# Kernel tuning notes

Measured on AMD Instinct MI355X. Metric: run time of the kernel, lower is better.

Reference implementation:

```python
import jax, jax.numpy as jnp
import numpy as np

N = 50000      # nodes
E = 1600000    # edges
F_IN = 128     # input_dim
H = 160        # hidden_dim
G = 512        # graphs in batch
C = 2          # num_classes
EPS = 1e-5     # BatchNorm eps


def setup_inputs() -> dict:
    key = jax.random.key(0)
    ks = jax.random.split(key, 12)
    x = jax.random.normal(ks[0], (N, F_IN), jnp.float32)
    edge_index = jax.random.randint(ks[1], (2, E), 0, N, dtype=jnp.int32)
    batch = jnp.sort(jax.random.randint(ks[2], (N,), 0, G, dtype=jnp.int32))

    def lin(k, fi, fo):
        s = 1.0 / np.sqrt(fi)
        kw, kb = jax.random.split(k)
        W = jax.random.uniform(kw, (fi, fo), jnp.float32, -s, s)
        b = jax.random.uniform(kb, (fo,), jnp.float32, -s, s)
        return W, b

    W1, b1 = lin(ks[3], F_IN, H)
    W2, b2 = lin(ks[4], H, H)
    W3, b3 = lin(ks[5], H, H)
    Wc1, bc1 = lin(ks[6], H, H // 2)
    Wc2, bc2 = lin(ks[7], H // 2, C)

    def bn(k):
        k1, k2, k3, k4 = jax.random.split(k, 4)
        gamma = jax.random.uniform(k1, (H,), jnp.float32, 0.5, 1.5)
        beta = jax.random.normal(k2, (H,), jnp.float32) * 0.1
        mean = jax.random.normal(k3, (H,), jnp.float32) * 0.1
        var = jax.random.uniform(k4, (H,), jnp.float32, 0.5, 1.5)
        return gamma, beta, mean, var

    g1, be1, m1, v1 = bn(ks[8])
    g2, be2, m2, v2 = bn(ks[9])
    g3, be3, m3, v3 = bn(ks[10])

    return dict(x=x, edge_index=edge_index, batch=batch,
                W1=W1, b1=b1, W2=W2, b2=b2, W3=W3, b3=b3,
                g1=g1, be1=be1, m1=m1, v1=v1,
                g2=g2, be2=be2, m2=m2, v2=v2,
                g3=g3, be3=be3, m3=m3, v3=v3,
                Wc1=Wc1, bc1=bc1, Wc2=Wc2, bc2=bc2)


def gcn_conv(x, W, b, src, dst):
    """PyG GCNConv: symmetric deg normalization with self-loops; lin -> aggregate -> +bias."""
    n = x.shape[0]
    h = x @ W                                   # [N, H]
    loop = jnp.arange(n, dtype=src.dtype)
    s = jnp.concatenate([src, loop])            # self-loops appended
    d = jnp.concatenate([dst, loop])
    deg = jax.ops.segment_sum(jnp.ones_like(d, jnp.float32), d, num_segments=n)
    inv = jnp.where(deg > 0, jax.lax.rsqrt(deg), 0.0)
    msg = h[s] * (inv[s] * inv[d])[:, None]     # [E+N, H] gather + norm
    return jax.ops.segment_sum(msg, d, num_segments=n) + b


def bn_eval(x, gamma, beta, mean, var):
    return (x - mean) * jax.lax.rsqrt(var + EPS) * gamma + beta


def reference(x, edge_index, batch, W1, b1, W2, b2, W3, b3,
              g1, be1, m1, v1, g2, be2, m2, v2, g3, be3, m3, v3,
              Wc1, bc1, Wc2, bc2):
    src, dst = edge_index[0], edge_index[1]
    # eval mode: dropout is identity, BN uses running stats
    h = jax.nn.relu(bn_eval(gcn_conv(x, W1, b1, src, dst), g1, be1, m1, v1))
    h = jax.nn.relu(bn_eval(gcn_conv(h, W2, b2, src, dst), g2, be2, m2, v2))
    h = jax.nn.relu(bn_eval(gcn_conv(h, W3, b3, src, dst), g3, be3, m3, v3))
    # global mean pool over graph ids
    sums = jax.ops.segment_sum(h, batch, num_segments=G)
    cnt = jax.ops.segment_sum(jnp.ones((h.shape[0],), jnp.float32), batch, num_segments=G)
    pooled = sums / jnp.clip(cnt, 1.0)[:, None]
    # MLP head
    z = jax.nn.relu(pooled @ Wc1 + bc1)
    return z @ Wc2 + bc2
```

## Files before the change

### kernel.cpp

```cpp
#include <hip/hip_runtime.h>

#define N_NODES   50000
#define N_EDGES   1600000
#define FDIM_IN   128
#define HDIM      160
#define N_GRAPHS  512
#define BN_EPS    1e-5f
#define NBKT_MAX  256
#define BKT_SH    8
#define HIST_BLOCKS 128

typedef short  frag8 __attribute__((ext_vector_type(8)));
typedef float  facc4 __attribute__((ext_vector_type(4)));


__device__ __forceinline__ unsigned short f2bf(float f) {
    unsigned int u = __float_as_uint(f);
    return (unsigned short)((u + 0x7FFFu + ((u >> 16) & 1u)) >> 16);
}

__device__ __forceinline__ unsigned int pack2(float lo, float hi) {
    return (unsigned int)f2bf(lo) | ((unsigned int)f2bf(hi) << 16);
}

__device__ __forceinline__ void addpk(float* acc, uint4 r) {
    acc[0] += __uint_as_float(r.x << 16);
    acc[1] += __uint_as_float(r.x & 0xFFFF0000u);
    acc[2] += __uint_as_float(r.y << 16);
    acc[3] += __uint_as_float(r.y & 0xFFFF0000u);
    acc[4] += __uint_as_float(r.z << 16);
    acc[5] += __uint_as_float(r.z & 0xFFFF0000u);
    acc[6] += __uint_as_float(r.w << 16);
    acc[7] += __uint_as_float(r.w & 0xFFFF0000u);
}


__global__ __launch_bounds__(256) void coarse_hist_kernel(const int* __restrict__ dst,
                                                          int* __restrict__ cg, int E) {
    __shared__ int h[NBKT_MAX];
    int tid = threadIdx.x;
    if (tid < NBKT_MAX) h[tid] = 0;
    __syncthreads();
    for (int e = blockIdx.x * 256 + tid; e < E; e += gridDim.x * 256)
        atomicAdd(&h[dst[e] >> BKT_SH], 1);
    __syncthreads();
    if (tid < NBKT_MAX) cg[blockIdx.x * NBKT_MAX + tid] = h[tid];
}


struct PrepArgs {
    const float *b, *g, *be, *m, *v;
    float *sc, *sh;
};

__global__ __launch_bounds__(256) void setup_kernel(const int* __restrict__ cg,
                                                    int* __restrict__ bucket_base,
                                                    int* __restrict__ bucket_cursor,
                                                    PrepArgs a0, PrepArgs a1, PrepArgs a2,
                                                    const float* __restrict__ W1,
                                                    const float* __restrict__ W2,
                                                    const float* __restrict__ W3,
                                                    unsigned short* __restrict__ o1,
                                                    unsigned short* __restrict__ o2,
                                                    unsigned short* __restrict__ o3) {
    int bid = blockIdx.x;
    int t = threadIdx.x;
    if (bid == 0) {
        __shared__ int h[NBKT_MAX];
        __shared__ int total;
        if (t < NBKT_MAX) {
            int s = 0;
            for (int b = 0; b < HIST_BLOCKS; ++b) s += cg[b * NBKT_MAX + t];
            h[t] = s;
        }
        __syncthreads();
        if (t == 0) {
            int run = 0;
            for (int i = 0; i < NBKT_MAX; ++i) { int c = h[i]; h[i] = run; run += c; }
            total = run;
        }
        __syncthreads();
        if (t < NBKT_MAX) {
            bucket_base[t] = h[t];
            bucket_cursor[t] = h[t];
        }
        if (t == 0) bucket_base[NBKT_MAX] = total;
    } else if (bid <= 3) {
        PrepArgs a = (bid == 1) ? a0 : (bid == 2) ? a1 : a2;
        if (t < HDIM) {
            float s = a.g[t] * rsqrtf(a.v[t] + BN_EPS);
            a.sc[t] = s;
            a.sh[t] = (a.b[t] - a.m[t]) * s + a.be[t];
        }
    } else {
        int i = (bid - 4) * 256 + t;
        const float* W;
        unsigned short* o;
        if (i < 128 * 160)                 { W = W1; o = o1; }
        else if (i < 128 * 160 + 160 * 160) { W = W2; o = o2; i -= 128 * 160; }
        else if (i < 128 * 160 + 2 * 160 * 160) { W = W3; o = o3; i -= 128 * 160 + 160 * 160; }
        else return;
        int j = i & 7;
        int l = (i >> 3) & 63;
        int u = (i >> 9) % 10;
        int tt = i / 5120;
        int k = tt * 32 + (l >> 4) * 8 + j;
        int nn = u * 16 + (l & 15);
        o[i] = f2bf(W[k * 160 + nn]);
    }
}

__global__ __launch_bounds__(256) void part_kernel(const int* __restrict__ src,
                                                   const int* __restrict__ dst,
                                                   int* __restrict__ bucket_cursor,
                                                   unsigned int* __restrict__ pairs, int E) {
    __shared__ int bcnt[NBKT_MAX], bbase[NBKT_MAX], lc[NBKT_MAX];
    int tid = threadIdx.x;
    int per = (E + gridDim.x - 1) / gridDim.x;
    int beg = blockIdx.x * per;
    int end = min(beg + per, E);
    if (tid < NBKT_MAX) { bcnt[tid] = 0; lc[tid] = 0; }
    __syncthreads();
    for (int e = beg + tid; e < end; e += 256)
        atomicAdd(&bcnt[dst[e] >> BKT_SH], 1);
    __syncthreads();
    if (tid < NBKT_MAX)
        bbase[tid] = bcnt[tid] ? atomicAdd(&bucket_cursor[tid], bcnt[tid]) : 0;
    __syncthreads();
    for (int e = beg + tid; e < end; e += 256) {
        int d = dst[e];
        int b = d >> BKT_SH;
        int pos = bbase[b] + atomicAdd(&lc[b], 1);
        pairs[pos] = ((unsigned int)src[e] << BKT_SH) | (unsigned int)(d & (NBKT_MAX - 1));
    }
}

__global__ __launch_bounds__(1024) void bucket_csr_kernel(const unsigned int* __restrict__ pairs,
                                                          const int* __restrict__ bucket_base,
                                                          int* __restrict__ row_off,
                                                          float* __restrict__ inv,
                                                          int* __restrict__ ssrc,
                                                          const float* __restrict__ x,
                                                          unsigned short* __restrict__ xs,
                                                          int n) {
    __shared__ int h[NBKT_MAX];
    __shared__ int ws[4];
    __shared__ float sinv[NBKT_MAX];
    int tid = threadIdx.x;
    int b = blockIdx.x;
    int node0 = b << BKT_SH;
    int beg = bucket_base[b], end = bucket_base[b + 1];
    if (tid < NBKT_MAX) h[tid] = 0;
    __syncthreads();
    for (int j = beg + tid; j < end; j += 1024)
        atomicAdd(&h[pairs[j] & (NBKT_MAX - 1)], 1);
    __syncthreads();
    int cntv = (tid < NBKT_MAX) ? h[tid] : 0;
    __syncthreads();
    int lane = tid & 63, wid = tid >> 6;
    int incl = cntv;
    #pragma unroll
    for (int off = 1; off < 64; off <<= 1) {
        int u = __shfl_up(incl, off);
        if (lane >= off) incl += u;
    }
    if (tid < NBKT_MAX && lane == 63) ws[wid] = incl;
    __syncthreads();
    if (tid == 0) {
        int r = 0;
        #pragma unroll
        for (int i = 0; i < 4; ++i) { int t = ws[i]; ws[i] = r; r += t; }
    }
    __syncthreads();
    int excl = (tid < NBKT_MAX) ? (ws[wid] + incl - cntv) : 0;
    if (tid < NBKT_MAX) {
        float iv = rsqrtf((float)(cntv + 1));
        int node = node0 + tid;
        if (node < n) {
            row_off[node] = beg + excl;
            inv[node] = iv;
        }
        sinv[tid] = iv;
        h[tid] = excl;
    }
    if (tid == 0 && (node0 + NBKT_MAX) >= n) row_off[n] = end;
    __syncthreads();
    for (int j = beg + tid; j < end; j += 1024) {
        unsigned int p = pairs[j];
        int pos = beg + atomicAdd(&h[p & (NBKT_MAX - 1)], 1);
        ssrc[pos] = (int)(p >> BKT_SH);
    }
    for (int idx = tid; idx < NBKT_MAX * 32; idx += 1024) {
        int nd = node0 + (idx >> 5);
        if (nd < n) {
            float w = sinv[idx >> 5];
            float4 v = ((const float4*)x)[(size_t)nd * 32 + (idx & 31)];
            ushort4 o;
            o.x = f2bf(v.x * w); o.y = f2bf(v.y * w);
            o.z = f2bf(v.z * w); o.w = f2bf(v.w * w);
            ((ushort4*)xs)[(size_t)nd * 32 + (idx & 31)] = o;
        }
    }
}


template <int C>
__global__ __launch_bounds__(256) void agg_grp_kernel(const unsigned short* __restrict__ in_s,
                                                      const float* __restrict__ inv,
                                                      const int* __restrict__ row_off,
                                                      const int* __restrict__ ssrc,
                                                      unsigned short* __restrict__ out, int n) {
    constexpr int LPR = C / 8;
    constexpr int G   = 64 / LPR;
    constexpr int RB  = C * 2;
    int wave = threadIdx.x >> 6;
    int lane = threadIdx.x & 63;
    int node = blockIdx.x * 4 + wave;
    if (node >= n) return;
    int g  = lane / LPR;
    int cl = lane - g * LPR;
    bool act = g < G;
    int beg = row_off[node], end = row_off[node + 1];
    const char* base = (const char*)in_s;
    int lb = cl * 16;

    float acc[8];
    #pragma unroll
    for (int i = 0; i < 8; ++i) acc[i] = 0.f;

    if (g == 0) {
        uint4 r = *(const uint4*)(base + (size_t)node * RB + lb);
        addpk(acc, r);
    }

    int e = act ? beg + g : end;
    for (; e + G < end; e += 2 * G) {
        int s0 = ssrc[e], s1 = ssrc[e + G];
        uint4 r0 = *(const uint4*)(base + (size_t)s0 * RB + lb);
        uint4 r1 = *(const uint4*)(base + (size_t)s1 * RB + lb);
        addpk(acc, r0);
        addpk(acc, r1);
    }
    if (e < end) {
        uint4 r = *(const uint4*)(base + (size_t)ssrc[e] * RB + lb);
        addpk(acc, r);
    }

    if (G == 4) {
        #pragma unroll
        for (int i = 0; i < 8; ++i) acc[i] += __shfl(acc[i], lane + 32);
        #pragma unroll
        for (int i = 0; i < 8; ++i) acc[i] += __shfl(acc[i], lane + 16);
    } else {
        #pragma unroll
        for (int i = 0; i < 8; ++i) {
            float a = __shfl(acc[i], lane + 20);
            float b = __shfl(acc[i], lane + 40);
            acc[i] += a + b;
        }
    }

    if (lane < LPR) {
        float wi = inv[node];
        uint4 o;
        o.x = pack2(acc[0] * wi, acc[1] * wi);
        o.y = pack2(acc[2] * wi, acc[3] * wi);
        o.z = pack2(acc[4] * wi, acc[5] * wi);
        o.w = pack2(acc[6] * wi, acc[7] * wi);
        *(uint4*)((char*)out + (size_t)node * RB + lb) = o;
    }
}


template <int K, int OUTMODE>
__global__ __launch_bounds__(256) void mfma_gemm_kernel(const unsigned short* __restrict__ A,
                                                        const unsigned short* __restrict__ Bp,
                                                        const float* __restrict__ sc,
                                                        const float* __restrict__ sh,
                                                        const float* __restrict__ inv,
                                                        float* __restrict__ CoutF,
                                                        unsigned short* __restrict__ CoutB,
                                                        int n) {
    constexpr int KT = K / 32;
    constexpr int BQ = K * 20;
    __shared__ uint4 Bs[BQ];
    int tid = threadIdx.x;
    for (int i = tid; i < BQ; i += 256) Bs[i] = ((const uint4*)Bp)[i];

    int wave = tid >> 6, lane = tid & 63;
    int m = lane & 15, q = lane >> 4;
    int row0 = blockIdx.x * 128 + wave * 16;
    int row1 = row0 + 64;

    int ar0 = row0 + m; ar0 = (ar0 < n) ? ar0 : (n - 1);
    int ar1 = row1 + m; ar1 = (ar1 < n) ? ar1 : (n - 1);
    const frag8* A0 = (const frag8*)(A + (size_t)ar0 * K);
    const frag8* A1 = (const frag8*)(A + (size_t)ar1 * K);
    const frag8* Bf = (const frag8*)Bs;

    facc4 acc0[10], acc1[10];
    #pragma unroll
    for (int u = 0; u < 10; ++u) {
        acc0[u] = (facc4){0.f, 0.f, 0.f, 0.f};
        acc1[u] = (facc4){0.f, 0.f, 0.f, 0.f};
    }

    __syncthreads();

    #pragma unroll
    for (int t = 0; t < KT; ++t) {
        frag8 af0 = A0[t * 4 + q];
        frag8 af1 = A1[t * 4 + q];
        #pragma unroll
        for (int u = 0; u < 10; ++u) {
            frag8 bf = Bf[(t * 10 + u) * 64 + lane];
            acc0[u] = __builtin_amdgcn_mfma_f32_16x16x32_bf16(af0, bf, acc0[u], 0, 0, 0);
            acc1[u] = __builtin_amdgcn_mfma_f32_16x16x32_bf16(af1, bf, acc1[u], 0, 0, 0);
        }
    }

    #pragma unroll
    for (int u = 0; u < 10; ++u) {
        int c = u * 16 + m;
        float scv = sc[c], shv = sh[c];
        #pragma unroll
        for (int r = 0; r < 4; ++r) {
            int rr = row0 + q * 4 + r;
            if (rr < n) {
                float v = fmaxf(acc0[u][r] * scv + shv, 0.f);
                if (OUTMODE == 1) CoutB[(size_t)rr * 160 + c] = f2bf(v * inv[rr]);
                else              CoutF[(size_t)rr * 160 + c] = v;
            }
            int rr1 = row1 + q * 4 + r;
            if (rr1 < n) {
                float v = fmaxf(acc1[u][r] * scv + shv, 0.f);
                if (OUTMODE == 1) CoutB[(size_t)rr1 * 160 + c] = f2bf(v * inv[rr1]);
                else              CoutF[(size_t)rr1 * 160 + c] = v;
            }
        }
    }
}


__global__ __launch_bounds__(256) void pool_head_kernel(const float* __restrict__ h,
                                                        const int* __restrict__ batch,
                                                        const float* __restrict__ Wc1,
                                                        const float* __restrict__ bc1,
                                                        const float* __restrict__ Wc2,
                                                        const float* __restrict__ bc2,
                                                        float* __restrict__ out, int n) {
    __shared__ float4 part[6][40];
    __shared__ float pooled[160];
    __shared__ float z[80];
    __shared__ int range[2];
    int g = blockIdx.x;
    int t = threadIdx.x;
    if (t < 2) {
        int target = g + t;
        int lo = 0, hi = n;
        while (lo < hi) {
            int mid = (lo + hi) >> 1;
            if (batch[mid] < target) lo = mid + 1; else hi = mid;
        }
        range[t] = lo;
    }
    __syncthreads();
    int lo = range[0], hi = range[1];
    int sub = t / 40, c4 = t - sub * 40;
    if (sub < 6) {
        float4 a = {0.f, 0.f, 0.f, 0.f};
        for (int r = lo + sub; r < hi; r += 6) {
            float4 v = ((const float4*)(h + (size_t)r * 160))[c4];
            a.x += v.x; a.y += v.y; a.z += v.z; a.w += v.w;
        }
        part[sub][c4] = a;
    }
    __syncthreads();
    if (t < 40) {
        float4 s = {0.f, 0.f, 0.f, 0.f};
        #pragma unroll
        for (int i = 0; i < 6; ++i) {
            float4 p = part[i][t];
            s.x += p.x; s.y += p.y; s.z += p.z; s.w += p.w;
        }
        float ic = 1.f / fmaxf((float)(hi - lo), 1.f);
        pooled[t * 4 + 0] = s.x * ic;
        pooled[t * 4 + 1] = s.y * ic;
        pooled[t * 4 + 2] = s.z * ic;
        pooled[t * 4 + 3] = s.w * ic;
    }
    __syncthreads();
    if (t < 80) {
        float s = bc1[t];
        for (int k = 0; k < 160; ++k) s += pooled[k] * Wc1[k * 80 + t];
        z[t] = fmaxf(s, 0.f);
    }
    __syncthreads();
    if (t < 2) {
        float s = bc2[t];
        for (int k = 0; k < 80; ++k) s += z[k] * Wc2[k * 2 + t];
        out[g * 2 + t] = s;
    }
}


static inline size_t align256(size_t x) { return (x + 255) & ~(size_t)255; }

extern "C" void kernel_launch(void* const* d_in, const int* in_sizes, int n_in,
                              void* d_out, int out_size, void* d_ws, size_t ws_size,
                              hipStream_t stream) {
    const float* x   = (const float*)d_in[0];
    const int* ei    = (const int*)d_in[1];
    const int* batch = (const int*)d_in[2];
    const float* W1  = (const float*)d_in[3];
    const float* b1  = (const float*)d_in[4];
    const float* W2  = (const float*)d_in[5];
    const float* b2  = (const float*)d_in[6];
    const float* W3  = (const float*)d_in[7];
    const float* b3  = (const float*)d_in[8];
    const float* g1  = (const float*)d_in[9];
    const float* be1 = (const float*)d_in[10];
    const float* m1  = (const float*)d_in[11];
    const float* v1  = (const float*)d_in[12];
    const float* g2  = (const float*)d_in[13];
    const float* be2 = (const float*)d_in[14];
    const float* m2  = (const float*)d_in[15];
    const float* v2  = (const float*)d_in[16];
    const float* g3  = (const float*)d_in[17];
    const float* be3 = (const float*)d_in[18];
    const float* m3  = (const float*)d_in[19];
    const float* v3  = (const float*)d_in[20];
    const float* Wc1 = (const float*)d_in[21];
    const float* bc1 = (const float*)d_in[22];
    const float* Wc2 = (const float*)d_in[23];
    const float* bc2 = (const float*)d_in[24];
    float* out = (float*)d_out;

    const int N = in_sizes[2];
    const int E = in_sizes[1] / 2;
    const int* src = ei;
    const int* dst = ei + E;

    char* w = (char*)d_ws;
    int*   row_off = (int*)w;             w += align256((size_t)(N + 1) * 4);
    float* inv     = (float*)w;           w += align256((size_t)N * 4);
    int*   ssrc    = (int*)w;             w += align256((size_t)E * 4);
    unsigned int* pairs = (unsigned int*)w; w += align256((size_t)E * 4);
    int*   cg      = (int*)w;             w += align256((size_t)HIST_BLOCKS * NBKT_MAX * 4);
    int*   bucket_base   = (int*)w;       w += align256((size_t)(NBKT_MAX + 1) * 4);
    int*   bucket_cursor = (int*)w;       w += align256((size_t)NBKT_MAX * 4);
    float* scsh    = (float*)w;           w += align256((size_t)6 * HDIM * 4);
    unsigned short* W1p = (unsigned short*)w;  w += align256((size_t)FDIM_IN * HDIM * 2);
    unsigned short* W2p = (unsigned short*)w;  w += align256((size_t)HDIM * HDIM * 2);
    unsigned short* W3p = (unsigned short*)w;  w += align256((size_t)HDIM * HDIM * 2);
    unsigned short* bufA_bf = (unsigned short*)w;  w += align256((size_t)N * HDIM * 2);
    char* regionR = w;
    unsigned short* xs_bf = (unsigned short*)regionR;
    unsigned short* hs_bf = (unsigned short*)(regionR + align256((size_t)N * FDIM_IN * 2));
    float* bufB = (float*)regionR;
    float* sc1 = scsh, *sh1 = scsh + 160, *sc2 = scsh + 320, *sh2 = scsh + 480,
         * sc3 = scsh + 640, *sh3 = scsh + 800;

    coarse_hist_kernel<<<HIST_BLOCKS, 256, 0, stream>>>(dst, cg, E);

    PrepArgs pa0 = {b1, g1, be1, m1, v1, sc1, sh1};
    PrepArgs pa1 = {b2, g2, be2, m2, v2, sc2, sh2};
    PrepArgs pa2 = {b3, g3, be3, m3, v3, sc3, sh3};
    int packTotal = 128 * 160 + 2 * 160 * 160;
    int setupBlocks = 4 + (packTotal + 255) / 256;
    setup_kernel<<<setupBlocks, 256, 0, stream>>>(cg, bucket_base, bucket_cursor,
                                                  pa0, pa1, pa2, W1, W2, W3, W1p, W2p, W3p);

    part_kernel<<<256, 256, 0, stream>>>(src, dst, bucket_cursor, pairs, E);
    int nbkt = (N + NBKT_MAX - 1) >> BKT_SH;
    bucket_csr_kernel<<<nbkt, 1024, 0, stream>>>(pairs, bucket_base, row_off, inv, ssrc, x, xs_bf, N);

    int gAgg = (N + 3) / 4;
    int gGemm = (N + 127) / 128;

    agg_grp_kernel<128><<<gAgg, 256, 0, stream>>>(xs_bf, inv, row_off, ssrc, bufA_bf, N);
    mfma_gemm_kernel<128, 1><<<gGemm, 256, 0, stream>>>(bufA_bf, W1p, sc1, sh1, inv, nullptr, hs_bf, N);
    agg_grp_kernel<160><<<gAgg, 256, 0, stream>>>(hs_bf, inv, row_off, ssrc, bufA_bf, N);
    mfma_gemm_kernel<160, 1><<<gGemm, 256, 0, stream>>>(bufA_bf, W2p, sc2, sh2, inv, nullptr, hs_bf, N);
    agg_grp_kernel<160><<<gAgg, 256, 0, stream>>>(hs_bf, inv, row_off, ssrc, bufA_bf, N);
    mfma_gemm_kernel<160, 0><<<gGemm, 256, 0, stream>>>(bufA_bf, W3p, sc3, sh3, inv, bufB, nullptr, N);

    pool_head_kernel<<<N_GRAPHS, 256, 0, stream>>>(bufB, batch, Wc1, bc1, Wc2, bc2, out, N);
}
```

Measured before the change: 459.3 us.

## Switch activations to fp16 with packed half accumulation and split aggregation launches

Activations and weights are now stored as fp16 instead of bf16. The gather-aggregation accumulates in packed half2 registers (v_pk_add_f16) rather than unpacking each element to fp32, and the GEMMs use the fp16 MFMA. Each aggregation launch is also split into two launches over node halves. The goal is to reduce ALU and register cost in the gather loop. The trade-off is fp16 overflow and precision risk when sums over high-degree rows are accumulated in half precision, plus one extra launch per layer.

```diff
diff --git a/kernel.cpp b/kernel.cpp
--- a/kernel.cpp
+++ b/kernel.cpp
@@ -10,28 +10,34 @@
 #define BKT_SH    8
 #define HIST_BLOCKS 128
 
-typedef short  frag8 __attribute__((ext_vector_type(8)));
+typedef _Float16 h2   __attribute__((ext_vector_type(2)));
+typedef _Float16 f16x8 __attribute__((ext_vector_type(8)));
 typedef float  facc4 __attribute__((ext_vector_type(4)));
 
 
-__device__ __forceinline__ unsigned short f2bf(float f) {
-    unsigned int u = __float_as_uint(f);
-    return (unsigned short)((u + 0x7FFFu + ((u >> 16) & 1u)) >> 16);
-}
-
-__device__ __forceinline__ unsigned int pack2(float lo, float hi) {
-    return (unsigned int)f2bf(lo) | ((unsigned int)f2bf(hi) << 16);
-}
-
-__device__ __forceinline__ void addpk(float* acc, uint4 r) {
-    acc[0] += __uint_as_float(r.x << 16);
-    acc[1] += __uint_as_float(r.x & 0xFFFF0000u);
-    acc[2] += __uint_as_float(r.y << 16);
-    acc[3] += __uint_as_float(r.y & 0xFFFF0000u);
-    acc[4] += __uint_as_float(r.z << 16);
-    acc[5] += __uint_as_float(r.z & 0xFFFF0000u);
-    acc[6] += __uint_as_float(r.w << 16);
-    acc[7] += __uint_as_float(r.w & 0xFFFF0000u);
+__device__ __forceinline__ unsigned short f2h_bits(float f) {
+    union { _Float16 h; unsigned short s; } c;
+    c.h = (_Float16)f;
+    return c.s;
+}
+
+__device__ __forceinline__ unsigned int pkh(float lo, float hi) {
+    return (unsigned int)f2h_bits(lo) | ((unsigned int)f2h_bits(hi) << 16);
+}
+
+__device__ __forceinline__ h2 u2h(unsigned int u) {
+    union { unsigned int u; h2 h; } c; c.u = u; return c.h;
+}
+
+__device__ __forceinline__ unsigned int h2u(h2 h) {
+    union { unsigned int u; h2 h; } c; c.h = h; return c.u;
+}
+
+__device__ __forceinline__ void addpk16(h2* acc, uint4 r) {
+    acc[0] += u2h(r.x);
+    acc[1] += u2h(r.y);
+    acc[2] += u2h(r.z);
+    acc[3] += u2h(r.w);
 }
 
 
@@ -106,7 +112,7 @@
         int tt = i / 5120;
         int k = tt * 32 + (l >> 4) * 8 + j;
         int nn = u * 16 + (l & 15);
-        o[i] = f2bf(W[k * 160 + nn]);
+        o[i] = f2h_bits(W[k * 160 + nn]);
     }
 }
 
@@ -196,8 +202,8 @@
             float w = sinv[idx >> 5];
             float4 v = ((const float4*)x)[(size_t)nd * 32 + (idx & 31)];
             ushort4 o;
-            o.x = f2bf(v.x * w); o.y = f2bf(v.y * w);
-            o.z = f2bf(v.z * w); o.w = f2bf(v.w * w);
+            o.x = f2h_bits(v.x * w); o.y = f2h_bits(v.y * w);
+            o.z = f2h_bits(v.z * w); o.w = f2h_bits(v.w * w);
             ((ushort4*)xs)[(size_t)nd * 32 + (idx & 31)] = o;
         }
     }
@@ -209,64 +215,65 @@
                                                       const float* __restrict__ inv,
                                                       const int* __restrict__ row_off,
                                                       const int* __restrict__ ssrc,
-                                                      unsigned short* __restrict__ out, int n) {
+                                                      unsigned short* __restrict__ out,
+                                                      int base, int n) {
     constexpr int LPR = C / 8;
     constexpr int G   = 64 / LPR;
     constexpr int RB  = C * 2;
     int wave = threadIdx.x >> 6;
     int lane = threadIdx.x & 63;
-    int node = blockIdx.x * 4 + wave;
+    int node = base + blockIdx.x * 4 + wave;
     if (node >= n) return;
     int g  = lane / LPR;
     int cl = lane - g * LPR;
     bool act = g < G;
     int beg = row_off[node], end = row_off[node + 1];
-    const char* base = (const char*)in_s;
+    const char* bptr = (const char*)in_s;
     int lb = cl * 16;
 
-    float acc[8];
+    h2 acc[4];
     #pragma unroll
-    for (int i = 0; i < 8; ++i) acc[i] = 0.f;
+    for (int i = 0; i < 4; ++i) acc[i] = (h2){(_Float16)0.f, (_Float16)0.f};
 
     if (g == 0) {
-        uint4 r = *(const uint4*)(base + (size_t)node * RB + lb);
-        addpk(acc, r);
+        uint4 r = *(const uint4*)(bptr + (size_t)node * RB + lb);
+        addpk16(acc, r);
     }
 
     int e = act ? beg + g : end;
     for (; e + G < end; e += 2 * G) {
         int s0 = ssrc[e], s1 = ssrc[e + G];
-        uint4 r0 = *(const uint4*)(base + (size_t)s0 * RB + lb);
-        uint4 r1 = *(const uint4*)(base + (size_t)s1 * RB + lb);
-        addpk(acc, r0);
-        addpk(acc, r1);
+        uint4 r0 = *(const uint4*)(bptr + (size_t)s0 * RB + lb);
+        uint4 r1 = *(const uint4*)(bptr + (size_t)s1 * RB + lb);
+        addpk16(acc, r0);
+        addpk16(acc, r1);
     }
     if (e < end) {
-        uint4 r = *(const uint4*)(base + (size_t)ssrc[e] * RB + lb);
-        addpk(acc, r);
+        uint4 r = *(const uint4*)(bptr + (size_t)ssrc[e] * RB + lb);
+        addpk16(acc, r);
     }
 
     if (G == 4) {
         #pragma unroll
-        for (int i = 0; i < 8; ++i) acc[i] += __shfl(acc[i], lane + 32);
-        #pragma unroll
-        for (int i = 0; i < 8; ++i) acc[i] += __shfl(acc[i], lane + 16);
+        for (int i = 0; i < 4; ++i) acc[i] += u2h(__shfl(h2u(acc[i]), lane + 32));
+        #pragma unroll
+        for (int i = 0; i < 4; ++i) acc[i] += u2h(__shfl(h2u(acc[i]), lane + 16));
     } else {
         #pragma unroll
-        for (int i = 0; i < 8; ++i) {
-            float a = __shfl(acc[i], lane + 20);
-            float b = __shfl(acc[i], lane + 40);
-            acc[i] += a + b;
+        for (int i = 0; i < 4; ++i) {
+            unsigned int ua = __shfl(h2u(acc[i]), lane + 20);
+            unsigned int ub = __shfl(h2u(acc[i]), lane + 40);
+            acc[i] += u2h(ua) + u2h(ub);
         }
     }
 
     if (lane < LPR) {
         float wi = inv[node];
         uint4 o;
-        o.x = pack2(acc[0] * wi, acc[1] * wi);
-        o.y = pack2(acc[2] * wi, acc[3] * wi);
-        o.z = pack2(acc[4] * wi, acc[5] * wi);
-        o.w = pack2(acc[6] * wi, acc[7] * wi);
+        o.x = pkh((float)acc[0].x * wi, (float)acc[0].y * wi);
+        o.y = pkh((float)acc[1].x * wi, (float)acc[1].y * wi);
+        o.z = pkh((float)acc[2].x * wi, (float)acc[2].y * wi);
+        o.w = pkh((float)acc[3].x * wi, (float)acc[3].y * wi);
         *(uint4*)((char*)out + (size_t)node * RB + lb) = o;
     }
 }
@@ -294,9 +301,9 @@
 
     int ar0 = row0 + m; ar0 = (ar0 < n) ? ar0 : (n - 1);
     int ar1 = row1 + m; ar1 = (ar1 < n) ? ar1 : (n - 1);
-    const frag8* A0 = (const frag8*)(A + (size_t)ar0 * K);
-    const frag8* A1 = (const frag8*)(A + (size_t)ar1 * K);
-    const frag8* Bf = (const frag8*)Bs;
+    const f16x8* A0 = (const f16x8*)(A + (size_t)ar0 * K);
+    const f16x8* A1 = (const f16x8*)(A + (size_t)ar1 * K);
+    const f16x8* Bf = (const f16x8*)Bs;
 
     facc4 acc0[10], acc1[10];
     #pragma unroll
@@ -309,13 +316,13 @@
 
     #pragma unroll
     for (int t = 0; t < KT; ++t) {
-        frag8 af0 = A0[t * 4 + q];
-        frag8 af1 = A1[t * 4 + q];
+        f16x8 af0 = A0[t * 4 + q];
+        f16x8 af1 = A1[t * 4 + q];
         #pragma unroll
         for (int u = 0; u < 10; ++u) {
-            frag8 bf = Bf[(t * 10 + u) * 64 + lane];
-            acc0[u] = __builtin_amdgcn_mfma_f32_16x16x32_bf16(af0, bf, acc0[u], 0, 0, 0);
-            acc1[u] = __builtin_amdgcn_mfma_f32_16x16x32_bf16(af1, bf, acc1[u], 0, 0, 0);
+            f16x8 bf = Bf[(t * 10 + u) * 64 + lane];
+            acc0[u] = __builtin_amdgcn_mfma_f32_16x16x32_f16(af0, bf, acc0[u], 0, 0, 0);
+            acc1[u] = __builtin_amdgcn_mfma_f32_16x16x32_f16(af1, bf, acc1[u], 0, 0, 0);
         }
     }
 
@@ -328,13 +335,13 @@
             int rr = row0 + q * 4 + r;
             if (rr < n) {
                 float v = fmaxf(acc0[u][r] * scv + shv, 0.f);
-                if (OUTMODE == 1) CoutB[(size_t)rr * 160 + c] = f2bf(v * inv[rr]);
+                if (OUTMODE == 1) CoutB[(size_t)rr * 160 + c] = f2h_bits(v * inv[rr]);
                 else              CoutF[(size_t)rr * 160 + c] = v;
             }
             int rr1 = row1 + q * 4 + r;
             if (rr1 < n) {
                 float v = fmaxf(acc1[u][r] * scv + shv, 0.f);
-                if (OUTMODE == 1) CoutB[(size_t)rr1 * 160 + c] = f2bf(v * inv[rr1]);
+                if (OUTMODE == 1) CoutB[(size_t)rr1 * 160 + c] = f2h_bits(v * inv[rr1]);
                 else              CoutF[(size_t)rr1 * 160 + c] = v;
             }
         }
@@ -475,14 +482,19 @@
     int nbkt = (N + NBKT_MAX - 1) >> BKT_SH;
     bucket_csr_kernel<<<nbkt, 1024, 0, stream>>>(pairs, bucket_base, row_off, inv, ssrc, x, xs_bf, N);
 
-    int gAgg = (N + 3) / 4;
+    int half = ((N / 2) + 3) & ~3;
+    int gA1 = half / 4;
+    int gA2 = (N - half + 3) / 4;
     int gGemm = (N + 127) / 128;
 
-    agg_grp_kernel<128><<<gAgg, 256, 0, stream>>>(xs_bf, inv, row_off, ssrc, bufA_bf, N);
+    agg_grp_kernel<128><<<gA1, 256, 0, stream>>>(xs_bf, inv, row_off, ssrc, bufA_bf, 0, half);
+    agg_grp_kernel<128><<<gA2, 256, 0, stream>>>(xs_bf, inv, row_off, ssrc, bufA_bf, half, N);
     mfma_gemm_kernel<128, 1><<<gGemm, 256, 0, stream>>>(bufA_bf, W1p, sc1, sh1, inv, nullptr, hs_bf, N);
-    agg_grp_kernel<160><<<gAgg, 256, 0, stream>>>(hs_bf, inv, row_off, ssrc, bufA_bf, N);
+    agg_grp_kernel<160><<<gA1, 256, 0, stream>>>(hs_bf, inv, row_off, ssrc, bufA_bf, 0, half);
+    agg_grp_kernel<160><<<gA2, 256, 0, stream>>>(hs_bf, inv, row_off, ssrc, bufA_bf, half, N);
     mfma_gemm_kernel<160, 1><<<gGemm, 256, 0, stream>>>(bufA_bf, W2p, sc2, sh2, inv, nullptr, hs_bf, N);
-    agg_grp_kernel<160><<<gAgg, 256, 0, stream>>>(hs_bf, inv, row_off, ssrc, bufA_bf, N);
+    agg_grp_kernel<160><<<gA1, 256, 0, stream>>>(hs_bf, inv, row_off, ssrc, bufA_bf, 0, half);
+    agg_grp_kernel<160><<<gA2, 256, 0, stream>>>(hs_bf, inv, row_off, ssrc, bufA_bf, half, N);
     mfma_gemm_kernel<160, 0><<<gGemm, 256, 0, stream>>>(bufA_bf, W3p, sc3, sh3, inv, bufB, nullptr, N);
 
     pool_head_kernel<<<N_GRAPHS, 256, 0, stream>>>(bufB, batch, Wc1, bc1, Wc2, bc2, out, N);
```

Result: slower. 480.0 us (+4.5%).
